# Optimization experiments

Hardware: AMD Instinct MI355X
Metric: run time of the kernel (lower is better)

## Reference

```python
import jax, jax.numpy as jnp
import numpy as np

ALPHA = 0.3
N_TAGS = 50  # POS tag vocabulary size (key space of the histogram)
B, S, R = 16, 160, 40


def setup_inputs() -> dict:
    key = jax.random.key(0)
    k1, k2, k3, k4, k5, k6 = jax.random.split(key, 6)
    return {
        "a_arc": jax.random.normal(k1, (B, S, S), dtype=jnp.float32),
        "a_rel": jax.random.normal(k2, (B, S, S, R), dtype=jnp.float32),
        "s_arc": jax.random.normal(k3, (B, S, S), dtype=jnp.float32),
        "s_rel": jax.random.normal(k4, (B, S, S, R), dtype=jnp.float32),
        "adds": jax.random.randint(k5, (B, S), 0, N_TAGS, dtype=jnp.int32),
        "pos": jax.random.randint(k6, (B, S), 0, N_TAGS, dtype=jnp.int32),
        "n_tags": N_TAGS,
    }


def reference(a_arc, a_rel, s_arc, s_rel, adds, pos, n_tags):
    # Histogram accumulation: score[(t1, t2)] += a_arc[i, p1, p2]
    # where t1 = adds[i, p1], t2 = adds[i, p2].  Flatten the pair key.
    R_ = a_rel.shape[-1]
    key_add = (adds[:, :, None] * n_tags + adds[:, None, :]).reshape(-1)  # [B*S*S]
    n_seg = n_tags * n_tags
    tab_arc = jax.ops.segment_sum(a_arc.reshape(-1), key_add, num_segments=n_seg)          # [T^2]
    tab_rel = jax.ops.segment_sum(a_rel.reshape(-1, R_), key_add, num_segments=n_seg)      # [T^2, R]
    # Gather back keyed on pos-tag pairs and blend with alpha.
    key_pos = pos[:, :, None] * n_tags + pos[:, None, :]  # [B, S, S]
    s_arc_out = s_arc + tab_arc[key_pos] * ALPHA
    s_rel_out = s_rel + tab_rel[key_pos] * ALPHA
    return s_arc_out, s_rel_out
```

## Files before the change

### kernel.cpp

```cpp
#include <hip/hip_runtime.h>

#define ALPHA 0.3f
#define NT    50
#define B_    16
#define S_    160
#define RR    40
#define Q_    (RR / 4)
#define NROW  (B_ * S_)
#define NPAIR (B_ * S_ * S_)
#define NSEG  (NT * NT)
#define NREL  (NPAIR * RR)
#define NCOL  (NT * RR + NT)
#define CW    2052

__global__ void zero_tab(float* __restrict__ tab, int n) {
    int i = blockIdx.x * blockDim.x + threadIdx.x;
    if (i < n) tab[i] = 0.0f;
}

__global__ void build_lists(const int* __restrict__ adds,
                            int* __restrict__ colstart,
                            int* __restrict__ collist) {
    __shared__ int tags[S_];
    __shared__ int cnt[NT];
    __shared__ int start[NT + 1];
    int b   = blockIdx.x;
    int tid = threadIdx.x;
    if (tid < S_) tags[tid] = adds[b * S_ + tid];
    __syncthreads();
    if (tid < NT) {
        int c = 0;
        for (int i = 0; i < S_; i++) c += (tags[i] == tid);
        cnt[tid] = c;
    }
    __syncthreads();
    if (tid == 0) {
        int s = 0;
        for (int t = 0; t < NT; t++) { start[t] = s; s += cnt[t]; }
        start[NT] = s;
    }
    __syncthreads();
    if (tid <= NT) colstart[b * 64 + tid] = start[tid];
    if (tid < NT) {
        int slot = start[tid];
        for (int i = 0; i < S_; i++)
            if (tags[i] == tid) collist[b * S_ + slot++] = i;
    }
}

template <int TO_C>
__global__ __launch_bounds__(256) void stage1(const float* __restrict__ a_arc,
                                              const float4* __restrict__ a_rel4,
                                              const int* __restrict__ adds,
                                              const int* __restrict__ colstart,
                                              const int* __restrict__ collist,
                                              float* __restrict__ C,
                                              float* __restrict__ tab_arc,
                                              float* __restrict__ tab_rel) {
    __shared__ int s_start[NT + 1];
    __shared__ int s_list[S_];
    int row = blockIdx.x;
    int b   = row / S_;
    int tid = threadIdx.x;
    if (tid <= NT) s_start[tid] = colstart[b * 64 + tid];
    if (tid < S_)  s_list[tid]  = collist[b * S_ + tid];
    __syncthreads();

    const float4* arow  = a_rel4 + (size_t)row * (S_ * Q_);
    const float*  aarow = a_arc + (size_t)row * S_;
    int t1 = TO_C ? 0 : adds[row];

    for (int cell = tid; cell < NT * Q_; cell += 256) {
        int t2 = cell / Q_;
        int q  = cell - t2 * Q_;
        float4 acc = make_float4(0.f, 0.f, 0.f, 0.f);
        int e1 = s_start[t2 + 1];
        for (int e = s_start[t2]; e < e1; ++e) {
            float4 v = arow[s_list[e] * Q_ + q];
            acc.x += v.x; acc.y += v.y; acc.z += v.z; acc.w += v.w;
        }
        if (TO_C) {
            ((float4*)(C + (size_t)row * CW))[cell] = acc;
        } else {
            float* dst = tab_rel + (size_t)t1 * (NT * RR) + cell * 4;
            atomicAdd(dst + 0, acc.x); atomicAdd(dst + 1, acc.y);
            atomicAdd(dst + 2, acc.z); atomicAdd(dst + 3, acc.w);
        }
    }
    if (tid < NT) {
        float acc = 0.f;
        int e1 = s_start[tid + 1];
        for (int e = s_start[tid]; e < e1; ++e) acc += aarow[s_list[e]];
        if (TO_C) C[(size_t)row * CW + NT * RR + tid] = acc;
        else      atomicAdd(tab_arc + t1 * NT + tid, acc);
    }
}

__global__ __launch_bounds__(256) void stage2(const float* __restrict__ C,
                                              const int* __restrict__ colstart,
                                              const int* __restrict__ collist,
                                              float* __restrict__ tab_arc,
                                              float* __restrict__ tab_rel) {
    int t1 = blockIdx.y;
    int c  = blockIdx.x * 256 + threadIdx.x;
    if (c >= NCOL) return;
    float acc = 0.f;
    for (int b = 0; b < B_; b++) {
        int s0 = colstart[b * 64 + t1], s1 = colstart[b * 64 + t1 + 1];
        for (int j = s0; j < s1; j++) {
            int row = b * S_ + collist[b * S_ + j];
            acc += C[(size_t)row * CW + c];
        }
    }
    if (c < NT * RR) tab_rel[t1 * (NT * RR) + c] = acc;
    else             tab_arc[t1 * NT + (c - NT * RR)] = acc;
}

__global__ __launch_bounds__(256) void apply_fused(const float* __restrict__ s_arc,
                                                   const float4* __restrict__ s_rel4,
                                                   const int* __restrict__ pos,
                                                   const float* __restrict__ tab_arc,
                                                   const float4* __restrict__ tab_rel4,
                                                   float* __restrict__ out_arc,
                                                   float4* __restrict__ out_rel4) {
    __shared__ int s_pos[S_];
    int row = blockIdx.x;
    int b   = row / S_;
    int p1  = row - b * S_;
    int tid = threadIdx.x;
    if (tid < S_) s_pos[tid] = pos[b * S_ + tid];
    __syncthreads();
    int base = s_pos[p1] * NT;

    const float4* srow = s_rel4   + (size_t)row * (S_ * Q_);
    float4*       orow = out_rel4 + (size_t)row * (S_ * Q_);
    for (int e = tid; e < S_ * Q_; e += 256) {
        int p2 = e / Q_;
        int q  = e - p2 * Q_;
        float4 sv = srow[e];
        float4 tv = tab_rel4[(base + s_pos[p2]) * Q_ + q];
        float4 o;
        o.x = sv.x + ALPHA * tv.x;
        o.y = sv.y + ALPHA * tv.y;
        o.z = sv.z + ALPHA * tv.z;
        o.w = sv.w + ALPHA * tv.w;
        orow[e] = o;
    }
    if (tid < S_) {
        out_arc[row * S_ + tid] = s_arc[row * S_ + tid]
                                + ALPHA * tab_arc[base + s_pos[tid]];
    }
}

extern "C" void kernel_launch(void* const* d_in, const int* in_sizes, int n_in,
                              void* d_out, int out_size, void* d_ws, size_t ws_size,
                              hipStream_t stream) {
    const float*  a_arc = (const float*)d_in[0];
    const float4* a_rel = (const float4*)d_in[1];
    const float*  s_arc = (const float*)d_in[2];
    const float4* s_rel = (const float4*)d_in[3];
    const int*    adds  = (const int*)d_in[4];
    const int*    pos   = (const int*)d_in[5];

    float* tab_arc  = (float*)d_ws;
    float* tab_rel  = tab_arc + NSEG;
    int*   colstart = (int*)(tab_rel + NSEG * RR);
    int*   collist  = colstart + B_ * 64;
    float* C        = (float*)(collist + B_ * S_);
    C = (float*)(((uintptr_t)C + 15) & ~(uintptr_t)15);

    size_t need_lists = (size_t)(NSEG * (RR + 1)) * 4
                      + (size_t)(B_ * 64 + B_ * S_) * 4 + 16;
    size_t need_full  = need_lists + (size_t)NROW * CW * 4;

    float*  out_arc = (float*)d_out;
    float4* out_rel = (float4*)(out_arc + NPAIR);

    const int BLK = 256;

    build_lists<<<B_, 192, 0, stream>>>(adds, colstart, collist);

    if (ws_size >= need_full) {
        stage1<1><<<NROW, 256, 0, stream>>>(a_arc, a_rel, adds, colstart, collist,
                                            C, nullptr, nullptr);
        dim3 g2((NCOL + 255) / 256, NT);
        stage2<<<g2, 256, 0, stream>>>(C, colstart, collist, tab_arc, tab_rel);
    } else {
        int n_tab = NSEG * (RR + 1);
        zero_tab<<<(n_tab + BLK - 1) / BLK, BLK, 0, stream>>>(tab_arc, n_tab);
        stage1<0><<<NROW, 256, 0, stream>>>(a_arc, a_rel, adds, colstart, collist,
                                            nullptr, tab_arc, tab_rel);
    }

    apply_fused<<<NROW, 256, 0, stream>>>(s_arc, s_rel, pos, tab_arc,
                                          (const float4*)tab_rel, out_arc, out_rel);
}
```

Measured before the change: 82.30 us.

## Flatten apply into grid-stride kernel and shrink stage1 blocks to 128 threads

Replaces the per-row apply kernel with a flat grid-stride kernel over all float4 elements of s_rel and s_arc, launched with a fixed grid of 2048 blocks. Per-thread index decode and pos lookups go through global memory instead of shared memory. This is meant to remove the tail inefficiency of 500 float4 per row split over 256 threads and to vectorize the arc path. Separately, stage1 now uses 128-thread blocks so fewer threads sit idle on its 500-cell loop, at the cost of more iterations per thread.

```diff
diff --git a/kernel.cpp b/kernel.cpp
--- a/kernel.cpp
+++ b/kernel.cpp
@@ -10,6 +10,8 @@
 #define NPAIR (B_ * S_ * S_)
 #define NSEG  (NT * NT)
 #define NREL  (NPAIR * RR)
+#define NREL4 (NPAIR * Q_)
+#define NARC4 (NPAIR / 4)
 #define NCOL  (NT * RR + NT)
 #define CW    2052
 
@@ -49,7 +51,7 @@
 }
 
 template <int TO_C>
-__global__ __launch_bounds__(256) void stage1(const float* __restrict__ a_arc,
+__global__ __launch_bounds__(128) void stage1(const float* __restrict__ a_arc,
                                               const float4* __restrict__ a_rel4,
                                               const int* __restrict__ adds,
                                               const int* __restrict__ colstart,
@@ -62,15 +64,15 @@
     int row = blockIdx.x;
     int b   = row / S_;
     int tid = threadIdx.x;
-    if (tid <= NT) s_start[tid] = colstart[b * 64 + tid];
-    if (tid < S_)  s_list[tid]  = collist[b * S_ + tid];
+    for (int i = tid; i <= NT; i += 128) s_start[i] = colstart[b * 64 + i];
+    for (int i = tid; i < S_; i += 128) s_list[i] = collist[b * S_ + i];
     __syncthreads();
 
     const float4* arow  = a_rel4 + (size_t)row * (S_ * Q_);
     const float*  aarow = a_arc + (size_t)row * S_;
     int t1 = TO_C ? 0 : adds[row];
 
-    for (int cell = tid; cell < NT * Q_; cell += 256) {
+    for (int cell = tid; cell < NT * Q_; cell += 128) {
         int t2 = cell / Q_;
         int q  = cell - t2 * Q_;
         float4 acc = make_float4(0.f, 0.f, 0.f, 0.f);
@@ -116,39 +118,49 @@
     else             tab_arc[t1 * NT + (c - NT * RR)] = acc;
 }
 
-__global__ __launch_bounds__(256) void apply_fused(const float* __restrict__ s_arc,
-                                                   const float4* __restrict__ s_rel4,
-                                                   const int* __restrict__ pos,
-                                                   const float* __restrict__ tab_arc,
-                                                   const float4* __restrict__ tab_rel4,
-                                                   float* __restrict__ out_arc,
-                                                   float4* __restrict__ out_rel4) {
-    __shared__ int s_pos[S_];
-    int row = blockIdx.x;
-    int b   = row / S_;
-    int p1  = row - b * S_;
-    int tid = threadIdx.x;
-    if (tid < S_) s_pos[tid] = pos[b * S_ + tid];
-    __syncthreads();
-    int base = s_pos[p1] * NT;
-
-    const float4* srow = s_rel4   + (size_t)row * (S_ * Q_);
-    float4*       orow = out_rel4 + (size_t)row * (S_ * Q_);
-    for (int e = tid; e < S_ * Q_; e += 256) {
-        int p2 = e / Q_;
-        int q  = e - p2 * Q_;
-        float4 sv = srow[e];
-        float4 tv = tab_rel4[(base + s_pos[p2]) * Q_ + q];
-        float4 o;
-        o.x = sv.x + ALPHA * tv.x;
-        o.y = sv.y + ALPHA * tv.y;
-        o.z = sv.z + ALPHA * tv.z;
-        o.w = sv.w + ALPHA * tv.w;
-        orow[e] = o;
-    }
-    if (tid < S_) {
-        out_arc[row * S_ + tid] = s_arc[row * S_ + tid]
-                                + ALPHA * tab_arc[base + s_pos[tid]];
+__global__ __launch_bounds__(256) void apply_flat(const float* __restrict__ s_arc,
+                                                  const float4* __restrict__ s_rel4,
+                                                  const int* __restrict__ pos,
+                                                  const float* __restrict__ tab_arc,
+                                                  const float4* __restrict__ tab_rel4,
+                                                  float* __restrict__ out_arc,
+                                                  float4* __restrict__ out_rel4) {
+    const int nthreads = gridDim.x * blockDim.x;
+    for (int t = blockIdx.x * blockDim.x + threadIdx.x;
+         t < NREL4 + NARC4; t += nthreads) {
+        if (t < NREL4) {
+            int pair = t / Q_;
+            int q    = t - pair * Q_;
+            int b    = pair / (S_ * S_);
+            int rem  = pair - b * (S_ * S_);
+            int p1   = rem / S_;
+            int p2   = rem - p1 * S_;
+            int key  = pos[b * S_ + p1] * NT + pos[b * S_ + p2];
+            float4 sv = s_rel4[t];
+            float4 tv = tab_rel4[key * Q_ + q];
+            float4 o;
+            o.x = sv.x + ALPHA * tv.x;
+            o.y = sv.y + ALPHA * tv.y;
+            o.z = sv.z + ALPHA * tv.z;
+            o.w = sv.w + ALPHA * tv.w;
+            out_rel4[t] = o;
+        } else {
+            int j   = t - NREL4;
+            int e0  = j * 4;
+            int b   = e0 / (S_ * S_);
+            int rem = e0 - b * (S_ * S_);
+            int p1  = rem / S_;
+            int p2  = rem - p1 * S_;
+            const int* posb = pos + b * S_;
+            int base = posb[p1] * NT;
+            float4 sv = ((const float4*)s_arc)[j];
+            float4 o;
+            o.x = sv.x + ALPHA * tab_arc[base + posb[p2 + 0]];
+            o.y = sv.y + ALPHA * tab_arc[base + posb[p2 + 1]];
+            o.z = sv.z + ALPHA * tab_arc[base + posb[p2 + 2]];
+            o.w = sv.w + ALPHA * tab_arc[base + posb[p2 + 3]];
+            ((float4*)out_arc)[j] = o;
+        }
     }
 }
 
@@ -181,17 +193,17 @@
     build_lists<<<B_, 192, 0, stream>>>(adds, colstart, collist);
 
     if (ws_size >= need_full) {
-        stage1<1><<<NROW, 256, 0, stream>>>(a_arc, a_rel, adds, colstart, collist,
+        stage1<1><<<NROW, 128, 0, stream>>>(a_arc, a_rel, adds, colstart, collist,
                                             C, nullptr, nullptr);
         dim3 g2((NCOL + 255) / 256, NT);
         stage2<<<g2, 256, 0, stream>>>(C, colstart, collist, tab_arc, tab_rel);
     } else {
         int n_tab = NSEG * (RR + 1);
         zero_tab<<<(n_tab + BLK - 1) / BLK, BLK, 0, stream>>>(tab_arc, n_tab);
-        stage1<0><<<NROW, 256, 0, stream>>>(a_arc, a_rel, adds, colstart, collist,
+        stage1<0><<<NROW, 128, 0, stream>>>(a_arc, a_rel, adds, colstart, collist,
                                             nullptr, tab_arc, tab_rel);
     }
 
-    apply_fused<<<NROW, 256, 0, stream>>>(s_arc, s_rel, pos, tab_arc,
-                                          (const float4*)tab_rel, out_arc, out_rel);
-}
+    apply_flat<<<2048, 256, 0, stream>>>(s_arc, s_rel, pos, tab_arc,
+                                         (const float4*)tab_rel, out_arc, out_rel);
+}
```

After: 83.40 us. About the same (+1.3%).

## Stage rows and table slices in LDS, use nontemporal stores in apply

Applied to the files above, without the earlier changes.

stage1 now loads each a_rel row with coalesced reads into LDS before the per-tag gather-sums, so the scattered per-tag global reads become LDS reads. The apply kernel preloads the 50x40 table slice for the row's pos tag into padded LDS and writes outputs with nontemporal stores. This targets uncoalesced global gathers and cache pollution from the streaming output, at the cost of more LDS per block (about 26KB in stage1), which lowers occupancy.

```diff
diff --git a/kernel.cpp b/kernel.cpp
--- a/kernel.cpp
+++ b/kernel.cpp
@@ -9,9 +9,11 @@
 #define NROW  (B_ * S_)
 #define NPAIR (B_ * S_ * S_)
 #define NSEG  (NT * NT)
-#define NREL  (NPAIR * RR)
+#define NREL4 (NPAIR * Q_)
 #define NCOL  (NT * RR + NT)
 #define CW    2052
+
+typedef float v4f __attribute__((ext_vector_type(4)));
 
 __global__ void zero_tab(float* __restrict__ tab, int n) {
     int i = blockIdx.x * blockDim.x + threadIdx.x;
@@ -57,17 +59,27 @@
                                               float* __restrict__ C,
                                               float* __restrict__ tab_arc,
                                               float* __restrict__ tab_rel) {
-    __shared__ int s_start[NT + 1];
-    __shared__ int s_list[S_];
+    __shared__ float4 a_lds[S_ * Q_];
+    __shared__ float4 aarc_lds[S_ / 4];
+    __shared__ int    s_start[NT + 1];
+    __shared__ int    s_list[S_];
     int row = blockIdx.x;
     int b   = row / S_;
     int tid = threadIdx.x;
-    if (tid <= NT) s_start[tid] = colstart[b * 64 + tid];
-    if (tid < S_)  s_list[tid]  = collist[b * S_ + tid];
-    __syncthreads();
-
-    const float4* arow  = a_rel4 + (size_t)row * (S_ * Q_);
-    const float*  aarow = a_arc + (size_t)row * S_;
+
+    for (int i = tid; i <= NT; i += 256) s_start[i] = colstart[b * 64 + i];
+    for (int i = tid; i < S_; i += 256)  s_list[i]  = collist[b * S_ + i];
+
+    const float4* arow = a_rel4 + (size_t)row * (S_ * Q_);
+#pragma unroll
+    for (int k = 0; k < 7; ++k) {
+        int idx = k * 256 + tid;
+        if (idx < S_ * Q_) a_lds[idx] = arow[idx];
+    }
+    if (tid < S_ / 4)
+        aarc_lds[tid] = ((const float4*)(a_arc + (size_t)row * S_))[tid];
+    __syncthreads();
+
     int t1 = TO_C ? 0 : adds[row];
 
     for (int cell = tid; cell < NT * Q_; cell += 256) {
@@ -76,7 +88,7 @@
         float4 acc = make_float4(0.f, 0.f, 0.f, 0.f);
         int e1 = s_start[t2 + 1];
         for (int e = s_start[t2]; e < e1; ++e) {
-            float4 v = arow[s_list[e] * Q_ + q];
+            float4 v = a_lds[s_list[e] * Q_ + q];
             acc.x += v.x; acc.y += v.y; acc.z += v.z; acc.w += v.w;
         }
         if (TO_C) {
@@ -88,9 +100,10 @@
         }
     }
     if (tid < NT) {
+        const float* aarcf = (const float*)aarc_lds;
         float acc = 0.f;
         int e1 = s_start[tid + 1];
-        for (int e = s_start[tid]; e < e1; ++e) acc += aarow[s_list[e]];
+        for (int e = s_start[tid]; e < e1; ++e) acc += aarcf[s_list[e]];
         if (TO_C) C[(size_t)row * CW + NT * RR + tid] = acc;
         else      atomicAdd(tab_arc + t1 * NT + tid, acc);
     }
@@ -116,39 +129,47 @@
     else             tab_arc[t1 * NT + (c - NT * RR)] = acc;
 }
 
-__global__ __launch_bounds__(256) void apply_fused(const float* __restrict__ s_arc,
-                                                   const float4* __restrict__ s_rel4,
-                                                   const int* __restrict__ pos,
-                                                   const float* __restrict__ tab_arc,
-                                                   const float4* __restrict__ tab_rel4,
-                                                   float* __restrict__ out_arc,
-                                                   float4* __restrict__ out_rel4) {
-    __shared__ int s_pos[S_];
+__global__ __launch_bounds__(256) void apply_v4(const float* __restrict__ s_arc,
+                                                const v4f* __restrict__ s_rel4,
+                                                const int* __restrict__ pos,
+                                                const float* __restrict__ tab_arc,
+                                                const v4f* __restrict__ tab_rel4,
+                                                float* __restrict__ out_arc,
+                                                v4f* __restrict__ out_rel4) {
+    __shared__ v4f   s_tab[NT][Q_ + 1];
+    __shared__ float s_tarc[NT];
+    __shared__ int   s_pos[S_];
     int row = blockIdx.x;
     int b   = row / S_;
     int p1  = row - b * S_;
     int tid = threadIdx.x;
+
+    int base = pos[b * S_ + p1] * NT;
+    for (int cell = tid; cell < NT * Q_; cell += 256) {
+        int t2 = cell / Q_;
+        int q  = cell - t2 * Q_;
+        s_tab[t2][q] = tab_rel4[(base + t2) * Q_ + q];
+    }
+    if (tid < NT) s_tarc[tid] = tab_arc[base + tid];
     if (tid < S_) s_pos[tid] = pos[b * S_ + tid];
     __syncthreads();
-    int base = s_pos[p1] * NT;
-
-    const float4* srow = s_rel4   + (size_t)row * (S_ * Q_);
-    float4*       orow = out_rel4 + (size_t)row * (S_ * Q_);
-    for (int e = tid; e < S_ * Q_; e += 256) {
-        int p2 = e / Q_;
-        int q  = e - p2 * Q_;
-        float4 sv = srow[e];
-        float4 tv = tab_rel4[(base + s_pos[p2]) * Q_ + q];
-        float4 o;
-        o.x = sv.x + ALPHA * tv.x;
-        o.y = sv.y + ALPHA * tv.y;
-        o.z = sv.z + ALPHA * tv.z;
-        o.w = sv.w + ALPHA * tv.w;
-        orow[e] = o;
+
+    const v4f* srow = s_rel4   + (size_t)row * (S_ * Q_);
+    v4f*       orow = out_rel4 + (size_t)row * (S_ * Q_);
+#pragma unroll
+    for (int k = 0; k < 7; ++k) {
+        int e = k * 256 + tid;
+        if (e < S_ * Q_) {
+            int p2 = e / Q_;
+            int q  = e - p2 * Q_;
+            v4f sv = srow[e];
+            v4f tv = s_tab[s_pos[p2]][q];
+            __builtin_nontemporal_store(sv + ALPHA * tv, orow + e);
+        }
     }
     if (tid < S_) {
-        out_arc[row * S_ + tid] = s_arc[row * S_ + tid]
-                                + ALPHA * tab_arc[base + s_pos[tid]];
+        float v = s_arc[(size_t)row * S_ + tid] + ALPHA * s_tarc[s_pos[tid]];
+        __builtin_nontemporal_store(v, out_arc + (size_t)row * S_ + tid);
     }
 }
 
@@ -158,7 +179,7 @@
     const float*  a_arc = (const float*)d_in[0];
     const float4* a_rel = (const float4*)d_in[1];
     const float*  s_arc = (const float*)d_in[2];
-    const float4* s_rel = (const float4*)d_in[3];
+    const v4f*    s_rel = (const v4f*)d_in[3];
     const int*    adds  = (const int*)d_in[4];
     const int*    pos   = (const int*)d_in[5];
 
@@ -173,8 +194,8 @@
                       + (size_t)(B_ * 64 + B_ * S_) * 4 + 16;
     size_t need_full  = need_lists + (size_t)NROW * CW * 4;
 
-    float*  out_arc = (float*)d_out;
-    float4* out_rel = (float4*)(out_arc + NPAIR);
+    float* out_arc = (float*)d_out;
+    v4f*   out_rel = (v4f*)(out_arc + NPAIR);
 
     const int BLK = 256;
 
@@ -192,6 +213,6 @@
                                             nullptr, tab_arc, tab_rel);
     }
 
-    apply_fused<<<NROW, 256, 0, stream>>>(s_arc, s_rel, pos, tab_arc,
-                                          (const float4*)tab_rel, out_arc, out_rel);
-}
+    apply_v4<<<NROW, 256, 0, stream>>>(s_arc, s_rel, pos, tab_arc,
+                                       (const v4f*)tab_rel, out_arc, out_rel);
+}
```

Measured after the change: 81.99 us. No clear change (-0.4%).
